# Performance work log

Measured on AMD Instinct MI355X. Metric: run time of the kernel, lower is better.

Reference implementation:

```python
import jax, jax.numpy as jnp
import numpy as np

NB, H, NH, R, C, V, B = 4, 256, 8, 20, 128, 32, 2
P = R * (R - 1) // 2  # 190 pairs


def _pair_matrix(rows):
    # each row of the mask has exactly two ones (a row pair); equals torch.combinations scatter
    i, j = np.triu_indices(rows, k=1)
    m = np.zeros((len(i), rows), np.float32)
    m[np.arange(len(i)), i] = 1.0
    m[np.arange(len(i)), j] = 1.0
    return jnp.asarray(m)


def setup_inputs() -> dict:
    key = jax.random.key(0)
    ks = jax.random.split(key, 16)

    def n(k, shape, s=0.02):
        return jax.random.normal(k, shape, jnp.float32) * s

    return {
        "tokens": jax.random.randint(ks[0], (B, R, C), 0, V, dtype=jnp.int32),
        "emb": n(ks[1], (V, H), 1.0),
        "ln1_g": jnp.ones((NB, H)), "ln1_b": jnp.zeros((NB, H)),
        "rWq": n(ks[2], (NB, H, H)), "rWk": n(ks[3], (NB, H, H)),
        "rWv": n(ks[4], (NB, H, H)), "rWo": n(ks[5], (NB, H, H)),
        "ln2_g": jnp.ones((NB, H)), "ln2_b": jnp.zeros((NB, H)),
        "cWq": n(ks[6], (NB, H, H)), "cWk": n(ks[7], (NB, H, H)),
        "cWv": n(ks[8], (NB, H, H)), "cWo": n(ks[9], (NB, H, H)),
        "ln3_g": jnp.ones((NB, H)), "ln3_b": jnp.zeros((NB, H)),
        "fW1": n(ks[10], (NB, H, 4 * H)), "fb1": jnp.zeros((NB, 4 * H)),
        "fW2": n(ks[11], (NB, 4 * H, H)), "fb2": jnp.zeros((NB, H)),
        "pW1": n(ks[12], (H, 4 * H)), "pb1": jnp.zeros((4 * H,)),
        "pW2": n(ks[13], (4 * H, 1)), "pb2": jnp.zeros((1,)),
        "uW": n(ks[14], (C, 1)), "ub": jnp.zeros((1,)),
    }


def _layernorm(x, g, b, eps=1e-5):
    m = x.mean(-1, keepdims=True)
    v = x.var(-1, keepdims=True)
    return (x - m) * jax.lax.rsqrt(v + eps) * g + b


def _attn(x, Wq, Wk, Wv, Wo):
    # x: [B, A, L, H]; multi-head attention over axis L
    b, a, l, h = x.shape
    d = h // NH
    q = (x @ Wq).reshape(b, a, l, NH, d)
    k = (x @ Wk).reshape(b, a, l, NH, d)
    v = (x @ Wv).reshape(b, a, l, NH, d)
    s = jnp.einsum('balhd,bamhd->bahlm', q, k) * (1.0 / float(np.sqrt(d)))
    p = jax.nn.softmax(s, axis=-1)
    o = jnp.einsum('bahlm,bamhd->balhd', p, v).reshape(b, a, l, h)
    return o @ Wo


def reference(tokens, emb, ln1_g, ln1_b, rWq, rWk, rWv, rWo, ln2_g, ln2_b, cWq, cWk, cWv, cWo, ln3_g, ln3_b, fW1, fb1, fW2, fb2, pW1, pb1, pW2, pb2, uW, ub):
    pm = _pair_matrix(tokens.shape[1])           # [P, R]
    x = emb[tokens]                              # [B, R, C, H]
    x = jnp.einsum('pr,brch->bpch', pm, x)       # pairwise row-sum -> [B, P, C, H]
    for i in range(ln1_g.shape[0]):
        h = _layernorm(x, ln1_g[i], ln1_b[i])
        x = x + _attn(h.swapaxes(1, 2), rWq[i], rWk[i], rWv[i], rWo[i]).swapaxes(1, 2)  # attend over pair axis
        h = _layernorm(x, ln2_g[i], ln2_b[i])
        x = x + _attn(h, cWq[i], cWk[i], cWv[i], cWo[i])                                # attend over column axis
        h = _layernorm(x, ln3_g[i], ln3_b[i])
        x = x + jax.nn.gelu(h @ fW1[i] + fb1[i]) @ fW2[i] + fb2[i]
    y = (jax.nn.gelu(x @ pW1 + pb1) @ pW2 + pb2).squeeze(-1)  # [B, P, C]
    y = (y @ uW + ub).squeeze(-1)                              # [B, P]
    return y
```

## Files before the change

kernel.cpp:

```cpp
#include <hip/hip_runtime.h>
#include <hip/hip_bf16.h>
#include <stdint.h>

#define NBLK   4
#define HDIM   256
#define NHEADS 8
#define RDIM   20
#define CDIM   128
#define PDIM   190
#define BDIM   2
#define FDIM   1024
#define NROWS  (BDIM*PDIM*CDIM)
#define NF     ((size_t)NROWS*(size_t)HDIM)
#define HROWS  (NROWS/2)

typedef __attribute__((ext_vector_type(8))) short bf16x8;
typedef __attribute__((ext_vector_type(4))) float f32x4;

__device__ __forceinline__ short f2b(float f){
    uint32_t u = __float_as_uint(f);
    u += 0x7fff + ((u >> 16) & 1);
    return (short)(u >> 16);
}
__device__ __forceinline__ float b2f(short s){
    return __uint_as_float(((uint32_t)(uint16_t)s) << 16);
}
__device__ __forceinline__ int cvtpk(float a, float b){
    int r;
    asm("v_cvt_pk_bf16_f32 %0, %1, %2" : "=v"(r) : "v"(a), "v"(b));
    return r;
}
__device__ __forceinline__ float gelu_fast(float x){
    const float tk0 = 1.5957691216057308f;
    const float k1  = 0.044715f;
    float u = tk0*(x + k1*x*x*x);
    return x / (1.0f + __expf(-u));
}
__device__ __forceinline__ void async16(const void* g, void* l){
    __builtin_amdgcn_global_load_lds(
        (const __attribute__((address_space(1))) void*)g,
        (__attribute__((address_space(3))) void*)l, 16, 0, 0);
}
__device__ __forceinline__ int xcd_swz(int nwg){
    int orig = blockIdx.x;
    int q = nwg >> 3, r = nwg & 7;
    int xcd = orig & 7, idx = orig >> 3;
    return ((xcd < r) ? xcd*(q+1) : r*(q+1) + (xcd - r)*q) + idx;
}

__global__ __launch_bounds__(256) void embed_ln_kernel(
    const int* __restrict__ tokens, const float* __restrict__ emb,
    const float* __restrict__ g, const float* __restrict__ bta,
    float* __restrict__ x, short* __restrict__ hb)
{
    int n    = blockIdx.x*4 + (threadIdx.x >> 6);
    int lane = threadIdx.x & 63;
    int c  = n % CDIM;
    int bp = n / CDIM;
    int p  = bp % PDIM;
    int b  = bp / PDIM;
    int i = 0, rem = p;
    while (rem >= (RDIM - 1 - i)) { rem -= (RDIM - 1 - i); ++i; }
    int j = i + 1 + rem;
    int t1 = tokens[(b*RDIM + i)*CDIM + c];
    int t2 = tokens[(b*RDIM + j)*CDIM + c];
    float4 e1 = *(const float4*)(emb + (size_t)t1*HDIM + lane*4);
    float4 e2 = *(const float4*)(emb + (size_t)t2*HDIM + lane*4);
    float4 v; v.x = e1.x+e2.x; v.y = e1.y+e2.y; v.z = e1.z+e2.z; v.w = e1.w+e2.w;
    *(float4*)(x + (size_t)n*HDIM + lane*4) = v;

    float s1 = v.x + v.y + v.z + v.w;
    float s2 = v.x*v.x + v.y*v.y + v.z*v.z + v.w*v.w;
    #pragma unroll
    for (int off = 1; off < 64; off <<= 1) {
        s1 += __shfl_xor(s1, off);
        s2 += __shfl_xor(s2, off);
    }
    float mu  = s1 * (1.0f/HDIM);
    float var = s2 * (1.0f/HDIM) - mu*mu;
    float inv = rsqrtf(var + 1e-5f);
    float4 gg = *(const float4*)(g   + lane*4);
    float4 bb = *(const float4*)(bta + lane*4);
    short4 o;
    o.x = f2b((v.x - mu)*inv*gg.x + bb.x);
    o.y = f2b((v.y - mu)*inv*gg.y + bb.y);
    o.z = f2b((v.z - mu)*inv*gg.z + bb.z);
    o.w = f2b((v.w - mu)*inv*gg.w + bb.w);
    *(short4*)(hb + (size_t)n*HDIM + lane*4) = o;
}

__global__ __launch_bounds__(256) void ln_kernel(
    const float* __restrict__ X, const float* __restrict__ g,
    const float* __restrict__ bta, short* __restrict__ Out)
{
    int row  = blockIdx.x*4 + (threadIdx.x >> 6);
    int lane = threadIdx.x & 63;
    float4 v = *(const float4*)(X + (size_t)row*HDIM + lane*4);
    float s1 = v.x + v.y + v.z + v.w;
    float s2 = v.x*v.x + v.y*v.y + v.z*v.z + v.w*v.w;
    #pragma unroll
    for (int off = 1; off < 64; off <<= 1) {
        s1 += __shfl_xor(s1, off);
        s2 += __shfl_xor(s2, off);
    }
    float mu  = s1 * (1.0f/HDIM);
    float var = s2 * (1.0f/HDIM) - mu*mu;
    float inv = rsqrtf(var + 1e-5f);
    float4 gg = *(const float4*)(g   + lane*4);
    float4 bb = *(const float4*)(bta + lane*4);
    short4 o;
    o.x = f2b((v.x - mu)*inv*gg.x + bb.x);
    o.y = f2b((v.y - mu)*inv*gg.y + bb.y);
    o.z = f2b((v.z - mu)*inv*gg.z + bb.z);
    o.w = f2b((v.w - mu)*inv*gg.w + bb.w);
    *(short4*)(Out + (size_t)row*HDIM + lane*4) = o;
}

__global__ __launch_bounds__(256) void tconv_kernel(
    const float* __restrict__ in, short* __restrict__ out,
    int K, int M, size_t inz, size_t outz)
{
    __shared__ float t[32][33];
    in  += (size_t)blockIdx.z * inz;
    out += (size_t)blockIdx.z * outz;
    int m0 = blockIdx.x*32, k0 = blockIdx.y*32;
    int r = threadIdx.x >> 5, c = threadIdx.x & 31;
    #pragma unroll
    for (int i = 0; i < 4; ++i)
        t[r + i*8][c] = in[(size_t)(k0 + r + i*8)*M + m0 + c];
    __syncthreads();
    #pragma unroll
    for (int i = 0; i < 4; ++i) {
        int rr = r + i*8;
        out[(size_t)(m0 + rr)*K + k0 + c] = f2b(t[c][rr]);
    }
}

template<int EPI>
__global__ __launch_bounds__(256) void mgemm_kernel(
    const short* __restrict__ A, const short* __restrict__ Wt,
    const float* __restrict__ bias,
    float* __restrict__ OutF,
    short* __restrict__ OB0, short* __restrict__ OB1, short* __restrict__ OB2,
    int K, int M, int ncol)
{
    __shared__ __align__(16) short smem[16384];
    short* As0 = smem;
    short* Bs0 = smem + 8192;
    const int tid  = threadIdx.x;
    const int lane = tid & 63, wid = tid >> 6;
    const int lq = lane & 15, lk = lane >> 4;
    const int wr = wid >> 1, wc = wid & 1;
    const int bid  = xcd_swz(gridDim.x);
    const int row0 = (bid / ncol) * 128, col0 = (bid % ncol) * 128;

    f32x4 acc[4][4] = {};

    auto stage = [&](int buf, int k0) {
        #pragma unroll
        for (int u = 0; u < 2; ++u) {
            int b   = wid*1024 + lane*16 + u*4096;
            int r   = b >> 6;
            int c16 = (b >> 4) & 3;
            int cs  = (c16 ^ ((r >> 1) & 3)) * 8;
            async16(A  + (size_t)(row0 + r)*K + k0 + cs, (char*)(As0 + buf*4096) + b);
            async16(Wt + (size_t)(col0 + r)*K + k0 + cs, (char*)(Bs0 + buf*4096) + b);
        }
    };

    stage(0, 0);
    const int NTK = K >> 5;
    for (int t = 0; t < NTK; ++t) {
        const int cur = t & 1;
        asm volatile("s_waitcnt vmcnt(0)" ::: "memory");
        __builtin_amdgcn_s_barrier();
        __builtin_amdgcn_sched_barrier(0);
        if (t + 1 < NTK) stage(cur ^ 1, (t + 1)*32);

        bf16x8 af[4], bfr[4];
        #pragma unroll
        for (int m = 0; m < 4; ++m) {
            int row = wr*64 + m*16 + lq;
            af[m] = *(const bf16x8*)((const char*)(As0 + cur*4096) + row*64 + ((lk ^ ((lq >> 1) & 3)) << 4));
        }
        #pragma unroll
        for (int n = 0; n < 4; ++n) {
            int row = wc*64 + n*16 + lq;
            bfr[n] = *(const bf16x8*)((const char*)(Bs0 + cur*4096) + row*64 + ((lk ^ ((lq >> 1) & 3)) << 4));
        }
        #pragma unroll
        for (int m = 0; m < 4; ++m)
            #pragma unroll
            for (int n = 0; n < 4; ++n)
                acc[m][n] = __builtin_amdgcn_mfma_f32_16x16x32_bf16(af[m], bfr[n], acc[m][n], 0, 0, 0);
    }

    if (EPI == 1 || EPI == 3) {
        const int rb  = row0 + wr*64 + (lk << 2);
        const int cb0 = col0 + wc*64 + lq;
        #pragma unroll
        for (int m = 0; m < 4; ++m)
            #pragma unroll
            for (int n = 0; n < 4; ++n) {
                int col = cb0 + n*16;
                #pragma unroll
                for (int r = 0; r < 4; ++r) {
                    int row = rb + m*16 + r;
                    float vv = acc[m][n][r];
                    if (EPI == 3) vv += bias[col];
                    OutF[(size_t)row*HDIM + col] += vv;
                }
            }
        return;
    }

    float bias8[4];
    if (EPI == 2 || EPI == 4) {
        #pragma unroll
        for (int n = 0; n < 4; ++n) bias8[n] = bias[col0 + wc*64 + n*16 + lq];
    }
    const int sec = col0 >> 8;
    const float qsc = (EPI == 0 && sec == 0) ? 0.2550540018992861f : 1.0f;

    __syncthreads();
    #pragma unroll
    for (int m = 0; m < 4; ++m) {
        #pragma unroll
        for (int n = 0; n < 4; ++n) {
            #pragma unroll
            for (int r = 0; r < 4; ++r) {
                int lrow = wr*64 + m*16 + lk*4 + r;
                int lcol = wc*64 + n*16 + lq;
                float vv = acc[m][n][r];
                if (EPI == 0) vv *= qsc;
                else if (EPI == 2) vv = gelu_fast(vv + bias8[n]);
                else {
                    int row = row0 + lrow, col = col0 + lcol;
                    float xo = OutF[(size_t)row*HDIM + col] + vv + bias8[n];
                    OutF[(size_t)row*HDIM + col] = xo;
                    vv = xo;
                }
                int byte = (lrow*256 + lcol*2) ^ ((lrow & 7) << 4);
                *(short*)((char*)smem + byte) = (short)cvtpk(vv, vv);
            }
        }
    }
    __syncthreads();

    short* obase;
    int ostride, ocol;
    if (EPI == 0) {
        obase = (sec == 0) ? OB0 : ((sec == 1) ? OB1 : OB2);
        ostride = HDIM; ocol = col0 & 255;
    } else if (EPI == 2) {
        obase = OB0; ostride = M; ocol = col0;
    } else {
        obase = OB0; ostride = HDIM; ocol = col0;
    }
    #pragma unroll
    for (int it = 0; it < 8; ++it) {
        int u    = it*256 + tid;
        int lrow = u >> 4;
        int uc   = u & 15;
        int su   = uc ^ (lrow & 7);
        int4 w = *(const int4*)((const char*)smem + lrow*256 + su*16);
        *(int4*)(obase + (size_t)(row0 + lrow)*ostride + ocol + uc*8) = w;
    }
}

template<int LP>
__global__ __launch_bounds__(256) void attn_mfma(
    const short* __restrict__ Q, const short* __restrict__ K,
    const short* __restrict__ V, short* __restrict__ O,
    int Lreal, int isRow)
{
    constexpr int NT  = LP/16;
    constexpr int NKT = LP/32;
    constexpr int NCH = LP/64;
    constexpr int LPB = LP*2;

    __shared__ short Ks[LP*32];
    __shared__ short Vt[32*LP];
    __shared__ short Ps[4*16*LP];

    const int bid  = xcd_swz(gridDim.x);
    const int head = bid & 7;
    size_t base; int S;
    if (isRow) {
        int c = (bid >> 3) & (CDIM-1);
        int b = bid >> 10;
        base = ((size_t)b*PDIM*CDIM + c)*HDIM + head*32;
        S = CDIM*HDIM;
    } else {
        int p = (bid >> 3) % PDIM;
        int b = bid / (8*PDIM);
        base = ((size_t)(b*PDIM + p)*CDIM)*HDIM + head*32;
        S = HDIM;
    }

    const int tid  = threadIdx.x;
    const int lane = tid & 63, wid = tid >> 6;
    const int lq = lane & 15, lk = lane >> 4;

    #pragma unroll
    for (int it = 0; it < LP/64; ++it) {
        int t16 = it*256 + tid;
        int row = t16 >> 2;
        int rc  = row < Lreal ? row : Lreal-1;
        int cs  = ((t16 & 3) ^ ((row >> 1) & 3)) * 8;
        async16(K + base + (size_t)rc*S + cs, (char*)Ks + (size_t)t16*16);
    }
    #pragma unroll
    for (int it = 0; it < LP/32; ++it) {
        int e   = it*256 + tid;
        int row = e >> 3;
        int d4  = (e & 7)*4;
        int rc  = row < Lreal ? row : Lreal-1;
        short4 v4 = *(const short4*)(V + base + (size_t)rc*S + d4);
        #pragma unroll
        for (int j = 0; j < 4; ++j) {
            int d = d4 + j;
            int off = ((d*LP + row)*2) ^ ((d & 7) << 4);
            *(short*)((char*)Vt + off) = ((const short*)&v4)[j];
        }
    }
    __syncthreads();

    char* pbase = (char*)Ps + wid*(16*LPB);
    const f32x4 zero = {0.f, 0.f, 0.f, 0.f};
    const bf16x8 ones = {(short)0x3F80,(short)0x3F80,(short)0x3F80,(short)0x3F80,
                         (short)0x3F80,(short)0x3F80,(short)0x3F80,(short)0x3F80};

    #pragma unroll 1
    for (int cc = 0; cc < NCH; ++cc) {
        const int chunk = wid + cc*4;
        const int qrow0 = chunk*16;

        int qr = qrow0 + lq; if (qr >= Lreal) qr = Lreal-1;
        bf16x8 qa = *(const bf16x8*)(Q + base + (size_t)qr*S + lk*8);

        f32x4 s[NT];
        #pragma unroll
        for (int t = 0; t < NT; ++t) {
            bf16x8 kb = *(const bf16x8*)((const char*)Ks + (t*16 + lq)*64 + ((lk ^ ((lq >> 1) & 3)) << 4));
            s[t] = __builtin_amdgcn_mfma_f32_16x16x32_bf16(qa, kb, zero, 0, 0, 0);
        }
        if ((NT-1)*16 + lq >= Lreal) {
            #pragma unroll
            for (int r = 0; r < 4; ++r) s[NT-1][r] = -1e30f;
        }

        #pragma unroll
        for (int t = 0; t < NT; ++t)
            #pragma unroll
            for (int r = 0; r < 4; ++r) {
                float p = exp2f(fminf(s[t][r], 126.f));
                int row = lk*4 + r, col = t*16 + lq;
                int off = (row*LPB + col*2) ^ ((row & 7) << 4);
                *(short*)(pbase + off) = (short)cvtpk(p, p);
            }
        asm volatile("s_waitcnt lgkmcnt(0)" ::: "memory");
        __builtin_amdgcn_sched_barrier(0);

        f32x4 acc0 = zero, acc1 = zero, accs = zero;
        #pragma unroll
        for (int kt = 0; kt < NKT; ++kt) {
            bf16x8 pa = *(const bf16x8*)(pbase + ((lq*LPB + kt*64 + lk*16) ^ ((lq & 7) << 4)));
            bf16x8 v0 = *(const bf16x8*)((char*)Vt + ((lq*LPB      + kt*64 + lk*16) ^ ((lq & 7) << 4)));
            bf16x8 v1 = *(const bf16x8*)((char*)Vt + (((16+lq)*LPB + kt*64 + lk*16) ^ ((lq & 7) << 4)));
            acc0 = __builtin_amdgcn_mfma_f32_16x16x32_bf16(pa, v0, acc0, 0, 0, 0);
            acc1 = __builtin_amdgcn_mfma_f32_16x16x32_bf16(pa, v1, acc1, 0, 0, 0);
            accs = __builtin_amdgcn_mfma_f32_16x16x32_bf16(pa, ones, accs, 0, 0, 0);
        }
        __builtin_amdgcn_sched_barrier(0);

        #pragma unroll
        for (int r = 0; r < 4; ++r) {
            int row = qrow0 + lk*4 + r;
            if (row < Lreal) {
                float inv = 1.0f / accs[r];
                O[base + (size_t)row*S + lq]      = (short)cvtpk(acc0[r]*inv, acc0[r]*inv);
                O[base + (size_t)row*S + 16 + lq] = (short)cvtpk(acc1[r]*inv, acc1[r]*inv);
            }
        }
    }
}

__global__ __launch_bounds__(256) void gemv_head(
    const short* __restrict__ T, const float* __restrict__ w,
    const float* __restrict__ bias, float* __restrict__ y)
{
    int row  = blockIdx.x*4 + (threadIdx.x >> 6);
    int lane = threadIdx.x & 63;
    const short* t = T + (size_t)row*FDIM;
    float acc = 0.f;
    #pragma unroll
    for (int it = 0; it < 4; ++it) {
        int ci = it*64 + lane;
        short4 tv = *(const short4*)(t + ci*4);
        float4 wv = *(const float4*)(w + ci*4);
        acc += b2f(tv.x)*wv.x + b2f(tv.y)*wv.y + b2f(tv.z)*wv.z + b2f(tv.w)*wv.w;
    }
    #pragma unroll
    for (int off = 1; off < 64; off <<= 1) acc += __shfl_xor(acc, off);
    if (lane == 0) y[row] = acc + bias[0];
}

__global__ __launch_bounds__(128) void final_kernel(
    const float* __restrict__ y, const float* __restrict__ uW,
    const float* __restrict__ ub, float* __restrict__ out)
{
    int bp = blockIdx.x;
    int c  = threadIdx.x;
    float v = y[(size_t)bp*CDIM + c]*uW[c];
    #pragma unroll
    for (int off = 1; off < 64; off <<= 1) v += __shfl_xor(v, off);
    __shared__ float r[2];
    if ((c & 63) == 0) r[c >> 6] = v;
    __syncthreads();
    if (c == 0) out[bp] = r[0] + r[1] + ub[0];
}

extern "C" void kernel_launch(void* const* d_in, const int* in_sizes, int n_in,
                              void* d_out, int out_size, void* d_ws, size_t ws_size,
                              hipStream_t stream)
{
    const int*   tokens = (const int*)  d_in[0];
    const float* emb    = (const float*)d_in[1];
    const float* ln1_g  = (const float*)d_in[2];
    const float* ln1_b  = (const float*)d_in[3];
    const float* rWq    = (const float*)d_in[4];
    const float* rWk    = (const float*)d_in[5];
    const float* rWv    = (const float*)d_in[6];
    const float* rWo    = (const float*)d_in[7];
    const float* ln2_g  = (const float*)d_in[8];
    const float* ln2_b  = (const float*)d_in[9];
    const float* cWq    = (const float*)d_in[10];
    const float* cWk    = (const float*)d_in[11];
    const float* cWv    = (const float*)d_in[12];
    const float* cWo    = (const float*)d_in[13];
    const float* ln3_g  = (const float*)d_in[14];
    const float* ln3_b  = (const float*)d_in[15];
    const float* fW1    = (const float*)d_in[16];
    const float* fb1    = (const float*)d_in[17];
    const float* fW2    = (const float*)d_in[18];
    const float* fb2    = (const float*)d_in[19];
    const float* pW1    = (const float*)d_in[20];
    const float* pb1    = (const float*)d_in[21];
    const float* pW2    = (const float*)d_in[22];
    const float* pb2    = (const float*)d_in[23];
    const float* uW     = (const float*)d_in[24];
    const float* ub     = (const float*)d_in[25];

    float* x  = (float*)d_ws;
    short* q  = (short*)(x + NF);
    short* k  = q + NF;
    short* v  = k + NF;
    short* hb = v + NF;
    float* y  = (float*)(hb + NF);
    short* wts = (short*)(y + NROWS);
    short* w_rqkv = wts;
    short* w_cqkv = w_rqkv + 4*768*256;
    short* w_ro   = w_cqkv + 4*768*256;
    short* w_co   = w_ro   + 4*256*256;
    short* w_f1   = w_co   + 4*256*256;
    short* w_f2   = w_f1   + (size_t)4*1024*256;
    short* w_p1   = w_f2   + (size_t)4*1024*256;
    short* tb = q;

    const size_t HH = 65536, HF = 262144, QZ = 768*256;

    tconv_kernel<<<dim3(8,8,NBLK),   256, 0, stream>>>(rWq, w_rqkv,          256, 256,  HH, QZ);
    tconv_kernel<<<dim3(8,8,NBLK),   256, 0, stream>>>(rWk, w_rqkv + 65536,  256, 256,  HH, QZ);
    tconv_kernel<<<dim3(8,8,NBLK),   256, 0, stream>>>(rWv, w_rqkv + 131072, 256, 256,  HH, QZ);
    tconv_kernel<<<dim3(8,8,NBLK),   256, 0, stream>>>(rWo, w_ro,            256, 256,  HH, HH);
    tconv_kernel<<<dim3(8,8,NBLK),   256, 0, stream>>>(cWq, w_cqkv,          256, 256,  HH, QZ);
    tconv_kernel<<<dim3(8,8,NBLK),   256, 0, stream>>>(cWk, w_cqkv + 65536,  256, 256,  HH, QZ);
    tconv_kernel<<<dim3(8,8,NBLK),   256, 0, stream>>>(cWv, w_cqkv + 131072, 256, 256,  HH, QZ);
    tconv_kernel<<<dim3(8,8,NBLK),   256, 0, stream>>>(cWo, w_co,            256, 256,  HH, HH);
    tconv_kernel<<<dim3(32,8,NBLK),  256, 0, stream>>>(fW1, w_f1,            256, 1024, HF, HF);
    tconv_kernel<<<dim3(8,32,NBLK),  256, 0, stream>>>(fW2, w_f2,            1024, 256, HF, HF);
    tconv_kernel<<<dim3(32,8,1),     256, 0, stream>>>(pW1, w_p1,            256, 1024, HF, HF);

    embed_ln_kernel<<<NROWS/4, 256, 0, stream>>>(tokens, emb, ln1_g, ln1_b, x, hb);

    const int gQKV = 6*(NROWS/128);
    const int gO   = 2*(NROWS/128);
    const int gF1  = 8*(HROWS/128);
    const int gF2  = 2*(HROWS/128);

    for (int i = 0; i < NBLK; ++i) {
        if (i > 0)
            ln_kernel<<<NROWS/4, 256, 0, stream>>>(x, ln1_g + i*HDIM, ln1_b + i*HDIM, hb);
        mgemm_kernel<0><<<gQKV, 256, 0, stream>>>(hb, w_rqkv + (size_t)i*QZ, nullptr, nullptr, q, k, v, 256, 768, 6);
        attn_mfma<192><<<BDIM*CDIM*NHEADS, 256, 0, stream>>>(q, k, v, hb, PDIM, 1);
        mgemm_kernel<1><<<gO, 256, 0, stream>>>(hb, w_ro + i*HH, nullptr, x, nullptr, nullptr, nullptr, 256, 256, 2);

        ln_kernel<<<NROWS/4, 256, 0, stream>>>(x, ln2_g + i*HDIM, ln2_b + i*HDIM, hb);
        mgemm_kernel<0><<<gQKV, 256, 0, stream>>>(hb, w_cqkv + (size_t)i*QZ, nullptr, nullptr, q, k, v, 256, 768, 6);
        attn_mfma<128><<<BDIM*PDIM*NHEADS, 256, 0, stream>>>(q, k, v, hb, CDIM, 0);
        mgemm_kernel<1><<<gO, 256, 0, stream>>>(hb, w_co + i*HH, nullptr, x, nullptr, nullptr, nullptr, 256, 256, 2);

        ln_kernel<<<NROWS/4, 256, 0, stream>>>(x, ln3_g + i*HDIM, ln3_b + i*HDIM, hb);
        for (int ch = 0; ch < 2; ++ch) {
            const size_t ro = (size_t)ch*HROWS*HDIM;
            mgemm_kernel<2><<<gF1, 256, 0, stream>>>(hb + ro, w_f1 + (size_t)i*HF,
                                                     fb1 + i*FDIM, nullptr, tb, nullptr, nullptr, 256, 1024, 8);
            if (i < NBLK-1)
                mgemm_kernel<3><<<gF2, 256, 0, stream>>>(tb, w_f2 + (size_t)i*HF,
                                                         fb2 + i*HDIM, x + ro,
                                                         nullptr, nullptr, nullptr, 1024, 256, 2);
            else
                mgemm_kernel<4><<<gF2, 256, 0, stream>>>(tb, w_f2 + (size_t)i*HF,
                                                         fb2 + i*HDIM, x + ro,
                                                         hb + ro, nullptr, nullptr, 1024, 256, 2);
        }
    }

    for (int ch = 0; ch < 2; ++ch) {
        const size_t ro = (size_t)ch*HROWS*HDIM;
        mgemm_kernel<2><<<gF1, 256, 0, stream>>>(hb + ro, w_p1, pb1, nullptr, tb, nullptr, nullptr, 256, 1024, 8);
        gemv_head<<<HROWS/4, 256, 0, stream>>>(tb, pW2, pb2, y + (size_t)ch*HROWS);
    }
    final_kernel<<<BDIM*PDIM, 128, 0, stream>>>(y, uW, ub, (float*)d_out);
}
```

Before: 1.440 ms.

## Fuse residual add and following LayerNorm into full-row output GEMM epilogues

Replaces the separate residual-update GEMMs and standalone LayerNorm kernels with a 512-thread GEMM that owns a full 128x256 output row tile. It adds the residual (and bias), writes x, computes row mean/variance with shuffles plus a shared-memory reduction, then writes the normalized bf16 activations directly. This removes three LayerNorm launches per block and the extra full read of x each one made. The cost is fewer, larger workgroups (half the grid for the O/F2 GEMMs) and more epilogue synchronization. The A tile is re-read as hb while hb is also the output, which is safe only because each block touches just its own rows.

Result: slower. 1.499 ms (+4.1%).

```diff
diff --git a/kernel.cpp b/kernel.cpp
--- a/kernel.cpp
+++ b/kernel.cpp
@@ -89,33 +89,6 @@
     *(short4*)(hb + (size_t)n*HDIM + lane*4) = o;
 }
 
-__global__ __launch_bounds__(256) void ln_kernel(
-    const float* __restrict__ X, const float* __restrict__ g,
-    const float* __restrict__ bta, short* __restrict__ Out)
-{
-    int row  = blockIdx.x*4 + (threadIdx.x >> 6);
-    int lane = threadIdx.x & 63;
-    float4 v = *(const float4*)(X + (size_t)row*HDIM + lane*4);
-    float s1 = v.x + v.y + v.z + v.w;
-    float s2 = v.x*v.x + v.y*v.y + v.z*v.z + v.w*v.w;
-    #pragma unroll
-    for (int off = 1; off < 64; off <<= 1) {
-        s1 += __shfl_xor(s1, off);
-        s2 += __shfl_xor(s2, off);
-    }
-    float mu  = s1 * (1.0f/HDIM);
-    float var = s2 * (1.0f/HDIM) - mu*mu;
-    float inv = rsqrtf(var + 1e-5f);
-    float4 gg = *(const float4*)(g   + lane*4);
-    float4 bb = *(const float4*)(bta + lane*4);
-    short4 o;
-    o.x = f2b((v.x - mu)*inv*gg.x + bb.x);
-    o.y = f2b((v.y - mu)*inv*gg.y + bb.y);
-    o.z = f2b((v.z - mu)*inv*gg.z + bb.z);
-    o.w = f2b((v.w - mu)*inv*gg.w + bb.w);
-    *(short4*)(Out + (size_t)row*HDIM + lane*4) = o;
-}
-
 __global__ __launch_bounds__(256) void tconv_kernel(
     const float* __restrict__ in, short* __restrict__ out,
     int K, int M, size_t inz, size_t outz)
@@ -140,7 +113,6 @@
 __global__ __launch_bounds__(256) void mgemm_kernel(
     const short* __restrict__ A, const short* __restrict__ Wt,
     const float* __restrict__ bias,
-    float* __restrict__ OutF,
     short* __restrict__ OB0, short* __restrict__ OB1, short* __restrict__ OB2,
     int K, int M, int ncol)
 {
@@ -195,27 +167,8 @@
                 acc[m][n] = __builtin_amdgcn_mfma_f32_16x16x32_bf16(af[m], bfr[n], acc[m][n], 0, 0, 0);
     }
 
-    if (EPI == 1 || EPI == 3) {
-        const int rb  = row0 + wr*64 + (lk << 2);
-        const int cb0 = col0 + wc*64 + lq;
-        #pragma unroll
-        for (int m = 0; m < 4; ++m)
-            #pragma unroll
-            for (int n = 0; n < 4; ++n) {
-                int col = cb0 + n*16;
-                #pragma unroll
-                for (int r = 0; r < 4; ++r) {
-                    int row = rb + m*16 + r;
-                    float vv = acc[m][n][r];
-                    if (EPI == 3) vv += bias[col];
-                    OutF[(size_t)row*HDIM + col] += vv;
-                }
-            }
-        return;
-    }
-
     float bias8[4];
-    if (EPI == 2 || EPI == 4) {
+    if (EPI == 2) {
         #pragma unroll
         for (int n = 0; n < 4; ++n) bias8[n] = bias[col0 + wc*64 + n*16 + lq];
     }
@@ -233,13 +186,7 @@
                 int lcol = wc*64 + n*16 + lq;
                 float vv = acc[m][n][r];
                 if (EPI == 0) vv *= qsc;
-                else if (EPI == 2) vv = gelu_fast(vv + bias8[n]);
-                else {
-                    int row = row0 + lrow, col = col0 + lcol;
-                    float xo = OutF[(size_t)row*HDIM + col] + vv + bias8[n];
-                    OutF[(size_t)row*HDIM + col] = xo;
-                    vv = xo;
-                }
+                else          vv = gelu_fast(vv + bias8[n]);
                 int byte = (lrow*256 + lcol*2) ^ ((lrow & 7) << 4);
                 *(short*)((char*)smem + byte) = (short)cvtpk(vv, vv);
             }
@@ -252,10 +199,8 @@
     if (EPI == 0) {
         obase = (sec == 0) ? OB0 : ((sec == 1) ? OB1 : OB2);
         ostride = HDIM; ocol = col0 & 255;
-    } else if (EPI == 2) {
+    } else {
         obase = OB0; ostride = M; ocol = col0;
-    } else {
-        obase = OB0; ostride = HDIM; ocol = col0;
     }
     #pragma unroll
     for (int it = 0; it < 8; ++it) {
@@ -265,6 +210,159 @@
         int su   = uc ^ (lrow & 7);
         int4 w = *(const int4*)((const char*)smem + lrow*256 + su*16);
         *(int4*)(obase + (size_t)(row0 + lrow)*ostride + ocol + uc*8) = w;
+    }
+}
+
+template<int MODE>
+__global__ __launch_bounds__(512) void mgemm_ln2(
+    const short* __restrict__ A, const short* __restrict__ Wt,
+    const float* __restrict__ bias,
+    float* __restrict__ X, short* __restrict__ HB,
+    const float* __restrict__ lng, const float* __restrict__ lnb, int K)
+{
+    __shared__ __align__(16) char smem[49152];
+    const int tid  = threadIdx.x;
+    const int lane = tid & 63, wid = tid >> 6;
+    const int lq = lane & 15, lk = lane >> 4;
+    const int wr = wid >> 2, wc = wid & 3;
+    const int bid  = xcd_swz(gridDim.x);
+    const int row0 = bid * 128;
+
+    f32x4 acc[4][4] = {};
+
+    auto stage = [&](int buf, int k0) {
+        char* base = smem + buf*24576;
+        {
+            int r = tid >> 2, c16 = tid & 3;
+            int cs = (c16 ^ ((r >> 1) & 3)) * 8;
+            async16(A + (size_t)(row0 + r)*K + k0 + cs, base + tid*16);
+        }
+        #pragma unroll
+        for (int p = 0; p < 2; ++p) {
+            int t16 = p*512 + tid;
+            int r = t16 >> 2, c16 = t16 & 3;
+            int cs = (c16 ^ ((r >> 1) & 3)) * 8;
+            async16(Wt + (size_t)r*K + k0 + cs, base + 8192 + t16*16);
+        }
+    };
+
+    stage(0, 0);
+    const int NTK = K >> 5;
+    for (int t = 0; t < NTK; ++t) {
+        const int cur = t & 1;
+        asm volatile("s_waitcnt vmcnt(0)" ::: "memory");
+        __builtin_amdgcn_s_barrier();
+        __builtin_amdgcn_sched_barrier(0);
+        if (t + 1 < NTK) stage(cur ^ 1, (t + 1)*32);
+
+        char* base = smem + cur*24576;
+        bf16x8 af[4], bfr[4];
+        #pragma unroll
+        for (int m = 0; m < 4; ++m) {
+            int row = wr*64 + m*16 + lq;
+            af[m] = *(const bf16x8*)(base + row*64 + ((lk ^ ((lq >> 1) & 3)) << 4));
+        }
+        #pragma unroll
+        for (int n = 0; n < 4; ++n) {
+            int row = wc*64 + n*16 + lq;
+            bfr[n] = *(const bf16x8*)(base + 8192 + row*64 + ((lk ^ ((lq >> 1) & 3)) << 4));
+        }
+        #pragma unroll
+        for (int m = 0; m < 4; ++m)
+            #pragma unroll
+            for (int n = 0; n < 4; ++n)
+                acc[m][n] = __builtin_amdgcn_mfma_f32_16x16x32_bf16(af[m], bfr[n], acc[m][n], 0, 0, 0);
+    }
+
+    float bias4[4];
+    if (MODE >= 1) {
+        #pragma unroll
+        for (int n = 0; n < 4; ++n) bias4[n] = bias[wc*64 + n*16 + lq];
+    }
+    float* red = (float*)smem;
+    __syncthreads();
+
+    #pragma unroll
+    for (int m = 0; m < 4; ++m) {
+        #pragma unroll
+        for (int r = 0; r < 4; ++r) {
+            int lrow = wr*64 + m*16 + lk*4 + r;
+            int grow = row0 + lrow;
+            float sa = 0.f, sq = 0.f;
+            #pragma unroll
+            for (int n = 0; n < 4; ++n) {
+                int col = wc*64 + n*16 + lq;
+                float xo = X[(size_t)grow*HDIM + col] + acc[m][n][r];
+                if (MODE >= 1) xo += bias4[n];
+                X[(size_t)grow*HDIM + col] = xo;
+                acc[m][n][r] = xo;
+                if (MODE < 2) { sa += xo; sq += xo*xo; }
+            }
+            if (MODE < 2) {
+                #pragma unroll
+                for (int off = 1; off < 16; off <<= 1) {
+                    sa += __shfl_xor(sa, off);
+                    sq += __shfl_xor(sq, off);
+                }
+                if (lq == 0) {
+                    red[(lrow*4 + wc)*2 + 0] = sa;
+                    red[(lrow*4 + wc)*2 + 1] = sq;
+                }
+            }
+        }
+    }
+    __syncthreads();
+
+    float g4[4], b4[4];
+    if (MODE < 2) {
+        #pragma unroll
+        for (int n = 0; n < 4; ++n) {
+            int col = wc*64 + n*16 + lq;
+            g4[n] = lng[col];
+            b4[n] = lnb[col];
+        }
+    }
+
+    char* cbuf = smem + 4096;
+    #pragma unroll
+    for (int h = 0; h < 2; ++h) {
+        if (wr == h) {
+            #pragma unroll
+            for (int m = 0; m < 4; ++m) {
+                #pragma unroll
+                for (int r = 0; r < 4; ++r) {
+                    int lr64 = m*16 + lk*4 + r;
+                    float mu = 0.f, inv = 0.f;
+                    if (MODE < 2) {
+                        int rr = h*64 + lr64;
+                        float s = red[(rr*4+0)*2] + red[(rr*4+1)*2] + red[(rr*4+2)*2] + red[(rr*4+3)*2];
+                        float q = red[(rr*4+0)*2+1] + red[(rr*4+1)*2+1] + red[(rr*4+2)*2+1] + red[(rr*4+3)*2+1];
+                        mu = s * (1.0f/HDIM);
+                        float var = q * (1.0f/HDIM) - mu*mu;
+                        inv = rsqrtf(var + 1e-5f);
+                    }
+                    #pragma unroll
+                    for (int n = 0; n < 4; ++n) {
+                        int lcol = wc*64 + n*16 + lq;
+                        float v = acc[m][n][r];
+                        if (MODE < 2) v = (v - mu)*inv*g4[n] + b4[n];
+                        int byte = (lr64*512 + lcol*2) ^ ((lr64 & 7) << 4);
+                        *(short*)(cbuf + byte) = (short)cvtpk(v, v);
+                    }
+                }
+            }
+        }
+        __syncthreads();
+        #pragma unroll
+        for (int it = 0; it < 4; ++it) {
+            int u    = it*512 + tid;
+            int lr64 = u >> 5;
+            int uc   = u & 31;
+            int su   = uc ^ (lr64 & 7);
+            int4 w = *(const int4*)(cbuf + lr64*512 + su*16);
+            *(int4*)(HB + (size_t)(row0 + h*64 + lr64)*HDIM + uc*8) = w;
+        }
+        __syncthreads();
     }
 }
 
@@ -485,41 +583,39 @@
     embed_ln_kernel<<<NROWS/4, 256, 0, stream>>>(tokens, emb, ln1_g, ln1_b, x, hb);
 
     const int gQKV = 6*(NROWS/128);
-    const int gO   = 2*(NROWS/128);
+    const int gOF  = NROWS/128;
     const int gF1  = 8*(HROWS/128);
-    const int gF2  = 2*(HROWS/128);
+    const int gF2  = HROWS/128;
 
     for (int i = 0; i < NBLK; ++i) {
-        if (i > 0)
-            ln_kernel<<<NROWS/4, 256, 0, stream>>>(x, ln1_g + i*HDIM, ln1_b + i*HDIM, hb);
-        mgemm_kernel<0><<<gQKV, 256, 0, stream>>>(hb, w_rqkv + (size_t)i*QZ, nullptr, nullptr, q, k, v, 256, 768, 6);
+        mgemm_kernel<0><<<gQKV, 256, 0, stream>>>(hb, w_rqkv + (size_t)i*QZ, nullptr, q, k, v, 256, 768, 6);
         attn_mfma<192><<<BDIM*CDIM*NHEADS, 256, 0, stream>>>(q, k, v, hb, PDIM, 1);
-        mgemm_kernel<1><<<gO, 256, 0, stream>>>(hb, w_ro + i*HH, nullptr, x, nullptr, nullptr, nullptr, 256, 256, 2);
-
-        ln_kernel<<<NROWS/4, 256, 0, stream>>>(x, ln2_g + i*HDIM, ln2_b + i*HDIM, hb);
-        mgemm_kernel<0><<<gQKV, 256, 0, stream>>>(hb, w_cqkv + (size_t)i*QZ, nullptr, nullptr, q, k, v, 256, 768, 6);
+        mgemm_ln2<0><<<gOF, 512, 0, stream>>>(hb, w_ro + i*HH, nullptr, x, hb,
+                                              ln2_g + i*HDIM, ln2_b + i*HDIM, 256);
+
+        mgemm_kernel<0><<<gQKV, 256, 0, stream>>>(hb, w_cqkv + (size_t)i*QZ, nullptr, q, k, v, 256, 768, 6);
         attn_mfma<128><<<BDIM*PDIM*NHEADS, 256, 0, stream>>>(q, k, v, hb, CDIM, 0);
-        mgemm_kernel<1><<<gO, 256, 0, stream>>>(hb, w_co + i*HH, nullptr, x, nullptr, nullptr, nullptr, 256, 256, 2);
-
-        ln_kernel<<<NROWS/4, 256, 0, stream>>>(x, ln3_g + i*HDIM, ln3_b + i*HDIM, hb);
+        mgemm_ln2<0><<<gOF, 512, 0, stream>>>(hb, w_co + i*HH, nullptr, x, hb,
+                                              ln3_g + i*HDIM, ln3_b + i*HDIM, 256);
+
         for (int ch = 0; ch < 2; ++ch) {
             const size_t ro = (size_t)ch*HROWS*HDIM;
             mgemm_kernel<2><<<gF1, 256, 0, stream>>>(hb + ro, w_f1 + (size_t)i*HF,
-                                                     fb1 + i*FDIM, nullptr, tb, nullptr, nullptr, 256, 1024, 8);
+                                                     fb1 + i*FDIM, tb, nullptr, nullptr, 256, 1024, 8);
             if (i < NBLK-1)
-                mgemm_kernel<3><<<gF2, 256, 0, stream>>>(tb, w_f2 + (size_t)i*HF,
-                                                         fb2 + i*HDIM, x + ro,
-                                                         nullptr, nullptr, nullptr, 1024, 256, 2);
+                mgemm_ln2<1><<<gF2, 512, 0, stream>>>(tb, w_f2 + (size_t)i*HF,
+                                                      fb2 + i*HDIM, x + ro, hb + ro,
+                                                      ln1_g + (i+1)*HDIM, ln1_b + (i+1)*HDIM, 1024);
             else
-                mgemm_kernel<4><<<gF2, 256, 0, stream>>>(tb, w_f2 + (size_t)i*HF,
-                                                         fb2 + i*HDIM, x + ro,
-                                                         hb + ro, nullptr, nullptr, 1024, 256, 2);
+                mgemm_ln2<2><<<gF2, 512, 0, stream>>>(tb, w_f2 + (size_t)i*HF,
+                                                      fb2 + i*HDIM, x + ro, hb + ro,
+                                                      nullptr, nullptr, 1024);
         }
     }
 
     for (int ch = 0; ch < 2; ++ch) {
         const size_t ro = (size_t)ch*HROWS*HDIM;
-        mgemm_kernel<2><<<gF1, 256, 0, stream>>>(hb + ro, w_p1, pb1, nullptr, tb, nullptr, nullptr, 256, 1024, 8);
+        mgemm_kernel<2><<<gF1, 256, 0, stream>>>(hb + ro, w_p1, pb1, tb, nullptr, nullptr, 256, 1024, 8);
         gemv_head<<<HROWS/4, 256, 0, stream>>>(tb, pW2, pb2, y + (size_t)ch*HROWS);
     }
     final_kernel<<<BDIM*PDIM, 128, 0, stream>>>(y, uW, ub, (float*)d_out);
```
